# Kernel optimization log

Measured on AMD Instinct MI355X. Metric: run time of the kernel, lower is better.

The kernel has to match this reference:

```python
import jax, jax.numpy as jnp
import numpy as np
from itertools import combinations

DILATIONS = [1, 2, 4, 8]
NUM_KERNELS = 84  # C(9,3)
KERNEL_LEN = 9


def setup_inputs() -> dict:
    key = jax.random.key(0)
    k_x, k_mask, k_bias, k_mean, k_std = jax.random.split(key, 5)
    B, L, C = 64, 2048, 8
    D = len(DILATIONS)
    F = 4  # features (biases) per kernel per dilation
    num_features = D * NUM_KERNELS * F

    # MiniRocket fixed kernels: -1 everywhere, +2 at each 3-index combination
    idx = np.asarray(list(combinations(range(KERNEL_LEN), 3)), dtype=np.int64)
    base = np.full((NUM_KERNELS, KERNEL_LEN), -1.0, dtype=np.float32)
    for i in range(NUM_KERNELS):
        base[i, idx[i]] = 2.0

    x = jax.random.normal(k_x, (B, L, C), dtype=jnp.float32)
    # binary channel masks per (dilation, kernel): which channels contribute
    channel_masks = (jax.random.uniform(k_mask, (D, NUM_KERNELS, C)) < 0.5).astype(jnp.float32)
    bias_matrices = jax.random.normal(k_bias, (D, NUM_KERNELS, F), dtype=jnp.float32)
    feature_mean = jax.random.normal(k_mean, (num_features,), dtype=jnp.float32)
    feature_std = jax.random.uniform(k_std, (num_features,), minval=0.5, maxval=1.5, dtype=jnp.float32)
    return {
        "x": x,
        "kernels": jnp.asarray(base),
        "channel_masks": channel_masks,
        "bias_matrices": bias_matrices,
        "feature_mean": feature_mean,
        "feature_std": feature_std,
    }


def _extract(x, kernels, channel_masks, bias_matrices):
    B, L, C = x.shape
    D, K, F = bias_matrices.shape
    x_cf = jnp.transpose(x, (0, 2, 1))  # [B, C, L]
    dtype = x.dtype
    t = jnp.arange(L)
    feats_all = []
    for d_idx, dil in enumerate(DILATIONS):
        pad = (KERNEL_LEN - 1) * dil // 2  # = 4*dil, so conv output length == L
        # Since the depthwise kernel is identical across channels for a given
        # kernel index, masked-channel-sum commutes with the conv:
        # response[b,k,:] = conv(sum_c mask[k,c] * x[b,c,:], kernel_k)
        mixed = jnp.einsum('kc,bcl->bkl', channel_masks[d_idx], x_cf)  # [B,K,L]
        resp = jax.lax.conv_general_dilated(
            mixed, kernels[:, None, :],
            window_strides=(1,), padding=[(pad, pad)],
            rhs_dilation=(dil,),
            dimension_numbers=('NCH', 'OIH', 'NCH'),
            feature_group_count=K,
        )  # [B, K, L]
        # PPV time-weights: kernels with odd (dilation_index + kernel_index)
        # are trimmed to the interior [pad, L-pad); others use the full length.
        should_trim = (pad > 0) and (L - 2 * pad > 0)
        interior = ((t >= pad) & (t < L - pad)).astype(dtype)  # [L]
        w_full = jnp.full((L,), 1.0 / L, dtype=dtype)
        w_trim = interior / jnp.asarray(L - 2 * pad, dtype=dtype)
        parity_odd = ((d_idx + jnp.arange(K)) % 2 == 1) & should_trim  # [K]
        w = jnp.where(parity_odd[:, None], w_trim[None, :], w_full[None, :])  # [K,L]
        # PPV: fraction of timesteps where response exceeds each bias
        ind = (resp[:, :, None, :] > bias_matrices[d_idx][None, :, :, None]).astype(dtype)  # [B,K,F,L]
        feats = jnp.einsum('bkfl,kl->bkf', ind, w)  # [B,K,F]
        feats_all.append(feats.reshape(B, K * F))
    return jnp.concatenate(feats_all, axis=1)  # [B, D*K*F]


def reference(x, kernels, channel_masks, bias_matrices, feature_mean, feature_std):
    flat = _extract(x, kernels, channel_masks, bias_matrices)
    return (flat - feature_mean) / feature_std
```

## Files before the change

### kernel.cpp

```cpp
#include <hip/hip_runtime.h>

#define TL 2048
#define TC 8
#define TK 84
#define TF 4
#define TD 4
#define ROWS 352
#define NFEAT (TD * TK * TF)
#define KF (TK * TF)
#define NQ 8

typedef unsigned int u32;
typedef __fp16 hf8 __attribute__((ext_vector_type(8)));
typedef float f32x4 __attribute__((ext_vector_type(4)));

__device__ __forceinline__ u32 pkrtz(float a, float b) {
    return __builtin_bit_cast(u32, __builtin_amdgcn_cvt_pkrtz(a, b));
}
__device__ __forceinline__ int swzrow(int e) { return e ^ ((e >> 3) & 7); }

__device__ __forceinline__ u32 red16(u32 v) {
    v += (u32)__builtin_amdgcn_update_dpp(0, (int)v, 0xB1,  0xF, 0xF, true);
    v += (u32)__builtin_amdgcn_update_dpp(0, (int)v, 0x4E,  0xF, 0xF, true);
    v += (u32)__builtin_amdgcn_update_dpp(0, (int)v, 0x141, 0xF, 0xF, true);
    v += (u32)__builtin_amdgcn_update_dpp(0, (int)v, 0x140, 0xF, 0xF, true);
    return v;
}

__global__ void mr_prep(const float* __restrict__ kern, const float* __restrict__ cmask,
                        uint4* __restrict__ A) {
    const int idx = blockIdx.x * 256 + threadIdx.x;
    if (idx >= TD * 18 * 64) return;
    const int lane = idx & 63, kbkt = (idx >> 6) % 18, d = idx / (18 * 64);
    const int kt = kbkt / 3, kb = kbkt % 3;
    const int col = lane & 15, lg = lane >> 4;
    const int k = kt * 16 + col, j = kb * 4 + lg;
    uint4 v = {0u, 0u, 0u, 0u};
    if (k < TK && j < 9) {
        const float wv = kern[k * 9 + j];
        const float* mp = cmask + ((size_t)d * TK + k) * TC;
        const float4 m0 = *(const float4*)mp;
        const float4 m1 = *(const float4*)(mp + 4);
        v.x = pkrtz(m0.x != 0.f ? wv : 0.f, m0.y != 0.f ? wv : 0.f);
        v.y = pkrtz(m0.z != 0.f ? wv : 0.f, m0.w != 0.f ? wv : 0.f);
        v.z = pkrtz(m1.x != 0.f ? wv : 0.f, m1.y != 0.f ? wv : 0.f);
        v.w = pkrtz(m1.z != 0.f ? wv : 0.f, m1.w != 0.f ? wv : 0.f);
    }
    A[idx] = v;
}

__global__ __launch_bounds__(256, 4) void mr_main(
    const float* __restrict__ x,
    const uint4* __restrict__ A,
    const float* __restrict__ bias,
    int* __restrict__ ws)
{
    __shared__ __align__(16) uint4 xh[ROWS];
    __shared__ __align__(16) float4 blds[TK];
    __shared__ u32 feats2[6][4][16];

    const int bx = blockIdx.x;
    const int q = bx & 7, d = (bx >> 3) & 3, b = bx >> 5;
    const int tid = threadIdx.x, lane = tid & 63, w = tid >> 6;
    const int dil = 1 << d, pad = 4 << d;
    const int t0 = q * 256;
    const float* xb = x + (size_t)b * TL * TC;

    if (tid < TK) blds[tid] = *(const float4*)(bias + ((size_t)d * TK + tid) * TF);

    for (int e = tid; e < ROWS; e += 256) {
        const int pos = t0 - 32 + e;
        uint4 v = {0u, 0u, 0u, 0u};
        if (pos >= 0 && pos < TL) {
            const float4* xp = (const float4*)(xb + (size_t)pos * TC);
            const float4 a = xp[0], h = xp[1];
            v.x = pkrtz(a.x, a.y); v.y = pkrtz(a.z, a.w);
            v.z = pkrtz(h.x, h.y); v.w = pkrtz(h.z, h.w);
        }
        xh[swzrow(e)] = v;
    }
    __syncthreads();

    const int col = lane & 15, lg = lane >> 4;
    const uint4* Ad = A + d * 18 * 64;

    hf8 bf[12];
    #pragma unroll
    for (int i = 0; i < 4; ++i)
        #pragma unroll
        for (int kb = 0; kb < 3; ++kb) {
            const int e = 32 + col - 4 * dil + (w * 4 + i) * 16 + (kb * 4 + lg) * dil;
            bf[i * 3 + kb] = __builtin_bit_cast(hf8, xh[swzrow(e)]);
        }

    bool interior[4];
    #pragma unroll
    for (int i = 0; i < 4; ++i) {
        const int tfirst = t0 + (w * 4 + i) * 16;
        interior[i] = (tfirst >= pad) && (tfirst + 16 <= TL - pad);
    }

    for (int kt = 0; kt < 6; ++kt) {
        hf8 af[3];
        #pragma unroll
        for (int kb = 0; kb < 3; ++kb)
            af[kb] = __builtin_bit_cast(hf8, Ad[(kt * 3 + kb) * 64 + lane]);

        float4 bq[4];
        #pragma unroll
        for (int rg = 0; rg < 4; ++rg) {
            int k = kt * 16 + lg * 4 + rg;
            k = (k < TK) ? k : (TK - 1);
            bq[rg] = blds[k];
        }

        u32 cnt[4] = {0u, 0u, 0u, 0u};

        #pragma unroll
        for (int i = 0; i < 4; ++i) {
            f32x4 C = {0.f, 0.f, 0.f, 0.f};
            #pragma unroll
            for (int kb = 0; kb < 3; ++kb)
                C = __builtin_amdgcn_mfma_f32_16x16x32_f16(af[kb], bf[i * 3 + kb], C, 0, 0, 0);

            if (interior[i]) {
                #pragma unroll
                for (int rg = 0; rg < 4; ++rg) {
                    const float cv = C[rg];
                    cnt[rg] += (cv > bq[rg].x) ? 0x1u : 0u;
                    cnt[rg] += (cv > bq[rg].y) ? 0x100u : 0u;
                    cnt[rg] += (cv > bq[rg].z) ? 0x10000u : 0u;
                    cnt[rg] += (cv > bq[rg].w) ? 0x1000000u : 0u;
                }
            } else {
                const int t = t0 + (w * 4 + i) * 16 + col;
                const bool ok = (t >= pad && t < TL - pad);
                #pragma unroll
                for (int rg = 0; rg < 4; ++rg) {
                    const float cv = C[rg];
                    const bool use = ((d ^ rg) & 1) ? ok : true;
                    cnt[rg] += (use && cv > bq[rg].x) ? 0x1u : 0u;
                    cnt[rg] += (use && cv > bq[rg].y) ? 0x100u : 0u;
                    cnt[rg] += (use && cv > bq[rg].z) ? 0x10000u : 0u;
                    cnt[rg] += (use && cv > bq[rg].w) ? 0x1000000u : 0u;
                }
            }
        }

        #pragma unroll
        for (int rg = 0; rg < 4; ++rg) cnt[rg] = red16(cnt[rg]);

        if (col == 0) {
            #pragma unroll
            for (int rg = 0; rg < 4; ++rg)
                feats2[kt][w][lg * 4 + rg] = cnt[rg];
        }
    }

    __syncthreads();
    for (int idx = tid; idx < KF; idx += 256) {
        const int k = idx >> 2, f = idx & 3;
        const int kt = k >> 4, r = k & 15;
        int cnt = 0;
        #pragma unroll
        for (int wv = 0; wv < 4; ++wv)
            cnt += (int)((feats2[kt][wv][r] >> (8 * f)) & 0xFFu);
        ws[(size_t)bx * KF + idx] = cnt;
    }
}

__global__ void mr_fin(const int* __restrict__ ws, const float* __restrict__ fmean,
                       const float* __restrict__ fstd, float* __restrict__ out) {
    const int o = blockIdx.x * 256 + threadIdx.x;
    const int fid = o % NFEAT, b = o / NFEAT;
    const int d = fid / KF, idx = fid % KF, k = idx >> 2;
    const int base = ((b * 32 + d * 8) * KF) + idx;
    int cnt = 0;
    #pragma unroll
    for (int q = 0; q < NQ; ++q) cnt += ws[base + q * KF];
    const float denom = ((d + k) & 1) ? (float)(TL - (8 << d)) : (float)TL;
    out[o] = ((float)cnt / denom - fmean[fid]) / fstd[fid];
}

extern "C" void kernel_launch(void* const* d_in, const int* in_sizes, int n_in,
                              void* d_out, int out_size, void* d_ws, size_t ws_size,
                              hipStream_t stream) {
    const float* x     = (const float*)d_in[0];
    const float* kern  = (const float*)d_in[1];
    const float* cmask = (const float*)d_in[2];
    const float* bias  = (const float*)d_in[3];
    const float* fmean = (const float*)d_in[4];
    const float* fstd  = (const float*)d_in[5];
    float* out = (float*)d_out;

    uint4* Aws = (uint4*)d_ws;
    int* cws = (int*)((char*)d_ws + TD * 18 * 64 * 16);

    hipLaunchKernelGGL(mr_prep, dim3((TD * 18 * 64 + 255) / 256), dim3(256), 0, stream,
                       kern, cmask, Aws);
    hipLaunchKernelGGL(mr_main, dim3(64 * TD * NQ), dim3(256), 0, stream,
                       x, Aws, bias, cws);
    hipLaunchKernelGGL(mr_fin, dim3(64 * NFEAT / 256), dim3(256), 0, stream,
                       cws, fmean, fstd, out);
}
```

Measured before the change: 35.82 us.

## Process all dilations per block over shorter time tiles to reuse staged input

Each block now loops over all four dilations on a 128-step time tile instead of handling one dilation on a 256-step tile. The fp16 input tile is loaded and converted once in LDS and reused across dilations, which removes the fourfold redundant global reads and conversions. Grid size drops from 2048 to 1024 blocks, and each block writes partial counts for all features. The finalize kernel now sums 16 time partitions per feature, so workspace traffic doubles.

```diff
diff --git a/kernel.cpp b/kernel.cpp
--- a/kernel.cpp
+++ b/kernel.cpp
@@ -5,10 +5,10 @@
 #define TK 84
 #define TF 4
 #define TD 4
-#define ROWS 352
+#define ROWS 224
 #define NFEAT (TD * TK * TF)
 #define KF (TK * TF)
-#define NQ 8
+#define NQ 16
 
 typedef unsigned int u32;
 typedef __fp16 hf8 __attribute__((ext_vector_type(8)));
@@ -56,17 +56,16 @@
     int* __restrict__ ws)
 {
     __shared__ __align__(16) uint4 xh[ROWS];
-    __shared__ __align__(16) float4 blds[TK];
-    __shared__ u32 feats2[6][4][16];
+    __shared__ __align__(16) float4 blds[KF];
+    __shared__ u32 feats2[TD][6][4][16];
 
     const int bx = blockIdx.x;
-    const int q = bx & 7, d = (bx >> 3) & 3, b = bx >> 5;
+    const int q = bx & 15, b = bx >> 4;
     const int tid = threadIdx.x, lane = tid & 63, w = tid >> 6;
-    const int dil = 1 << d, pad = 4 << d;
-    const int t0 = q * 256;
+    const int t0 = q * 128;
     const float* xb = x + (size_t)b * TL * TC;
 
-    if (tid < TK) blds[tid] = *(const float4*)(bias + ((size_t)d * TK + tid) * TF);
+    for (int i2 = tid; i2 < KF; i2 += 256) blds[i2] = ((const float4*)bias)[i2];
 
     for (int e = tid; e < ROWS; e += 256) {
         const int pos = t0 - 32 + e;
@@ -82,90 +81,95 @@
     __syncthreads();
 
     const int col = lane & 15, lg = lane >> 4;
-    const uint4* Ad = A + d * 18 * 64;
-
-    hf8 bf[12];
-    #pragma unroll
-    for (int i = 0; i < 4; ++i)
+
+    for (int d = 0; d < TD; ++d) {
+        const int dil = 1 << d, pad = 4 << d;
+        const uint4* Ad = A + d * 18 * 64;
+
+        hf8 bf[6];
         #pragma unroll
-        for (int kb = 0; kb < 3; ++kb) {
-            const int e = 32 + col - 4 * dil + (w * 4 + i) * 16 + (kb * 4 + lg) * dil;
-            bf[i * 3 + kb] = __builtin_bit_cast(hf8, xh[swzrow(e)]);
+        for (int i = 0; i < 2; ++i)
+            #pragma unroll
+            for (int kb = 0; kb < 3; ++kb) {
+                const int e = 32 + col - 4 * dil + (w * 2 + i) * 16 + (kb * 4 + lg) * dil;
+                bf[i * 3 + kb] = __builtin_bit_cast(hf8, xh[swzrow(e)]);
+            }
+
+        bool interior[2];
+        #pragma unroll
+        for (int i = 0; i < 2; ++i) {
+            const int tfirst = t0 + (w * 2 + i) * 16;
+            interior[i] = (tfirst >= pad) && (tfirst + 16 <= TL - pad);
         }
 
-    bool interior[4];
-    #pragma unroll
-    for (int i = 0; i < 4; ++i) {
-        const int tfirst = t0 + (w * 4 + i) * 16;
-        interior[i] = (tfirst >= pad) && (tfirst + 16 <= TL - pad);
-    }
-
-    for (int kt = 0; kt < 6; ++kt) {
-        hf8 af[3];
-        #pragma unroll
-        for (int kb = 0; kb < 3; ++kb)
-            af[kb] = __builtin_bit_cast(hf8, Ad[(kt * 3 + kb) * 64 + lane]);
-
-        float4 bq[4];
-        #pragma unroll
-        for (int rg = 0; rg < 4; ++rg) {
-            int k = kt * 16 + lg * 4 + rg;
-            k = (k < TK) ? k : (TK - 1);
-            bq[rg] = blds[k];
+        for (int kt = 0; kt < 6; ++kt) {
+            hf8 af[3];
+            #pragma unroll
+            for (int kb = 0; kb < 3; ++kb)
+                af[kb] = __builtin_bit_cast(hf8, Ad[(kt * 3 + kb) * 64 + lane]);
+
+            float4 bq[4];
+            #pragma unroll
+            for (int rg = 0; rg < 4; ++rg) {
+                int k = kt * 16 + lg * 4 + rg;
+                k = (k < TK) ? k : (TK - 1);
+                bq[rg] = blds[d * TK + k];
+            }
+
+            u32 cnt[4] = {0u, 0u, 0u, 0u};
+
+            #pragma unroll
+            for (int i = 0; i < 2; ++i) {
+                f32x4 C = {0.f, 0.f, 0.f, 0.f};
+                C = __builtin_amdgcn_mfma_f32_16x16x32_f16(af[0], bf[i * 3 + 0], C, 0, 0, 0);
+                C = __builtin_amdgcn_mfma_f32_16x16x32_f16(af[1], bf[i * 3 + 1], C, 0, 0, 0);
+                C = __builtin_amdgcn_mfma_f32_16x16x32_f16(af[2], bf[i * 3 + 2], C, 0, 0, 0);
+
+                if (interior[i]) {
+                    #pragma unroll
+                    for (int rg = 0; rg < 4; ++rg) {
+                        const float cv = C[rg];
+                        cnt[rg] += (cv > bq[rg].x) ? 0x1u : 0u;
+                        cnt[rg] += (cv > bq[rg].y) ? 0x100u : 0u;
+                        cnt[rg] += (cv > bq[rg].z) ? 0x10000u : 0u;
+                        cnt[rg] += (cv > bq[rg].w) ? 0x1000000u : 0u;
+                    }
+                } else {
+                    const int t = t0 + (w * 2 + i) * 16 + col;
+                    const bool ok = (t >= pad && t < TL - pad);
+                    #pragma unroll
+                    for (int rg = 0; rg < 4; ++rg) {
+                        const float cv = C[rg];
+                        const bool use = ((d ^ rg) & 1) ? ok : true;
+                        cnt[rg] += (use && cv > bq[rg].x) ? 0x1u : 0u;
+                        cnt[rg] += (use && cv > bq[rg].y) ? 0x100u : 0u;
+                        cnt[rg] += (use && cv > bq[rg].z) ? 0x10000u : 0u;
+                        cnt[rg] += (use && cv > bq[rg].w) ? 0x1000000u : 0u;
+                    }
+                }
+            }
+
+            #pragma unroll
+            for (int rg = 0; rg < 4; ++rg) cnt[rg] = red16(cnt[rg]);
+
+            if (col == 0) {
+                #pragma unroll
+                for (int rg = 0; rg < 4; ++rg)
+                    feats2[d][kt][w][lg * 4 + rg] = cnt[rg];
+            }
         }
-
-        u32 cnt[4] = {0u, 0u, 0u, 0u};
-
-        #pragma unroll
-        for (int i = 0; i < 4; ++i) {
-            f32x4 C = {0.f, 0.f, 0.f, 0.f};
-            #pragma unroll
-            for (int kb = 0; kb < 3; ++kb)
-                C = __builtin_amdgcn_mfma_f32_16x16x32_f16(af[kb], bf[i * 3 + kb], C, 0, 0, 0);
-
-            if (interior[i]) {
-                #pragma unroll
-                for (int rg = 0; rg < 4; ++rg) {
-                    const float cv = C[rg];
-                    cnt[rg] += (cv > bq[rg].x) ? 0x1u : 0u;
-                    cnt[rg] += (cv > bq[rg].y) ? 0x100u : 0u;
-                    cnt[rg] += (cv > bq[rg].z) ? 0x10000u : 0u;
-                    cnt[rg] += (cv > bq[rg].w) ? 0x1000000u : 0u;
-                }
-            } else {
-                const int t = t0 + (w * 4 + i) * 16 + col;
-                const bool ok = (t >= pad && t < TL - pad);
-                #pragma unroll
-                for (int rg = 0; rg < 4; ++rg) {
-                    const float cv = C[rg];
-                    const bool use = ((d ^ rg) & 1) ? ok : true;
-                    cnt[rg] += (use && cv > bq[rg].x) ? 0x1u : 0u;
-                    cnt[rg] += (use && cv > bq[rg].y) ? 0x100u : 0u;
-                    cnt[rg] += (use && cv > bq[rg].z) ? 0x10000u : 0u;
-                    cnt[rg] += (use && cv > bq[rg].w) ? 0x1000000u : 0u;
-                }
-            }
-        }
-
-        #pragma unroll
-        for (int rg = 0; rg < 4; ++rg) cnt[rg] = red16(cnt[rg]);
-
-        if (col == 0) {
-            #pragma unroll
-            for (int rg = 0; rg < 4; ++rg)
-                feats2[kt][w][lg * 4 + rg] = cnt[rg];
-        }
     }
 
     __syncthreads();
-    for (int idx = tid; idx < KF; idx += 256) {
-        const int k = idx >> 2, f = idx & 3;
+    for (int idx = tid; idx < NFEAT; idx += 256) {
+        const int d2 = idx / KF, rem = idx % KF;
+        const int k = rem >> 2, f = rem & 3;
         const int kt = k >> 4, r = k & 15;
         int cnt = 0;
         #pragma unroll
         for (int wv = 0; wv < 4; ++wv)
-            cnt += (int)((feats2[kt][wv][r] >> (8 * f)) & 0xFFu);
-        ws[(size_t)bx * KF + idx] = cnt;
+            cnt += (int)((feats2[d2][kt][wv][r] >> (8 * f)) & 0xFFu);
+        ws[(size_t)bx * NFEAT + idx] = cnt;
     }
 }
 
@@ -173,11 +177,11 @@
                        const float* __restrict__ fstd, float* __restrict__ out) {
     const int o = blockIdx.x * 256 + threadIdx.x;
     const int fid = o % NFEAT, b = o / NFEAT;
-    const int d = fid / KF, idx = fid % KF, k = idx >> 2;
-    const int base = ((b * 32 + d * 8) * KF) + idx;
+    const int d = fid / KF, k = (fid % KF) >> 2;
+    const size_t base = (size_t)b * NQ * NFEAT + fid;
     int cnt = 0;
     #pragma unroll
-    for (int q = 0; q < NQ; ++q) cnt += ws[base + q * KF];
+    for (int q = 0; q < NQ; ++q) cnt += ws[base + (size_t)q * NFEAT];
     const float denom = ((d + k) & 1) ? (float)(TL - (8 << d)) : (float)TL;
     out[o] = ((float)cnt / denom - fmean[fid]) / fstd[fid];
 }
@@ -198,7 +202,7 @@
 
     hipLaunchKernelGGL(mr_prep, dim3((TD * 18 * 64 + 255) / 256), dim3(256), 0, stream,
                        kern, cmask, Aws);
-    hipLaunchKernelGGL(mr_main, dim3(64 * TD * NQ), dim3(256), 0, stream,
+    hipLaunchKernelGGL(mr_main, dim3(64 * NQ), dim3(256), 0, stream,
                        x, Aws, bias, cws);
     hipLaunchKernelGGL(mr_fin, dim3(64 * NFEAT / 256), dim3(256), 0, stream,
                        cws, fmean, fstd, out);
```

After: 40.87 us. 1.14x slower.
